# Performance work log

Hardware: AMD Instinct MI355X
Metric: run time of the kernel (lower is better)

## Reference

```python
import jax, jax.numpy as jnp
import numpy as np
from jax import lax

NEG = -1e30  # safe -inf surrogate (avoids nan grads)
CTC_WEIGHT = 0.3


def _excl_cumsum(e):
    # exclusive cumsum along last axis: (..., U) -> (..., U+1)
    c = jnp.cumsum(e, axis=-1)
    return jnp.concatenate([jnp.zeros_like(c[..., :1]), c], axis=-1)


def _rnnt_loss(log_probs, targets, frame_len, tgt_len, blank):
    """RNNT forward DP. log_probs: (B,T,U+1,V) log-softmaxed. Returns per-seq NLL (B,)."""
    B, T, U1, V = log_probs.shape
    blank_lp = log_probs[..., blank]  # (B,T,U1)
    emit = jnp.take_along_axis(log_probs[:, :, :U1 - 1, :],
                               targets[:, None, :, None], axis=3)[..., 0]  # (B,T,U)
    # alpha[0,u] = sum_{j<u} emit[0,j]
    alpha0 = _excl_cumsum(emit[:, 0])  # (B,U1)

    def step(alpha_prev, inp):
        blank_prev, emit_t = inp  # (B,U1), (B,U)
        a = alpha_prev + blank_prev
        # alpha[t,u] = LSE(a_u, alpha[t,u-1] + emit[t,u-1]) solved in closed form:
        # alpha[t,u] = E[u] + cumLSE_{k<=u}(a_k - E[k]),  E = exclusive cumsum of emit
        E = _excl_cumsum(emit_t)
        alpha_t = E + lax.associative_scan(jnp.logaddexp, a - E, axis=-1)
        return alpha_t, alpha_t

    xs = (jnp.swapaxes(blank_lp[:, :-1], 0, 1), jnp.swapaxes(emit[:, 1:], 0, 1))
    _, alphas = lax.scan(step, alpha0, xs)
    alphas = jnp.concatenate([alpha0[None], alphas], axis=0)  # (T,B,U1)
    bi = jnp.arange(B)
    t_idx = frame_len - 1
    ll = alphas[t_idx, bi, tgt_len] + blank_lp[bi, t_idx, tgt_len]
    return -ll


def _ctc_loss(log_probs, targets, frame_len, tgt_len, blank):
    """CTC forward DP. log_probs: (B,T,V) log-softmaxed. Returns per-seq NLL (B,)."""
    B, T, V = log_probs.shape
    U = targets.shape[1]
    S = 2 * U + 1
    ext = jnp.full((B, S), blank, dtype=targets.dtype).at[:, 1::2].set(targets)  # (B,S)
    lp_ext = jnp.take_along_axis(log_probs, ext[:, None, :], axis=2)  # (B,T,S)
    ext_m2 = jnp.pad(ext[:, :-2], ((0, 0), (2, 0)), constant_values=blank)
    can_skip = (jnp.arange(S)[None, :] >= 2) & (ext != blank) & (ext != ext_m2)
    alpha0 = jnp.full((B, S), NEG).at[:, 0].set(lp_ext[:, 0, 0]).at[:, 1].set(lp_ext[:, 0, 1])

    def step(alpha, lp_t):
        p1 = jnp.pad(alpha[:, :-1], ((0, 0), (1, 0)), constant_values=NEG)
        p2 = jnp.where(can_skip,
                       jnp.pad(alpha[:, :-2], ((0, 0), (2, 0)), constant_values=NEG), NEG)
        m = jnp.maximum(jnp.maximum(alpha, p1), p2)
        new = lp_t + m + jnp.log(jnp.exp(alpha - m) + jnp.exp(p1 - m) + jnp.exp(p2 - m))
        return new, new

    _, alphas = lax.scan(step, alpha0, jnp.swapaxes(lp_ext, 0, 1)[1:])
    alphas = jnp.concatenate([alpha0[None], alphas], axis=0)  # (T,B,S)
    bi = jnp.arange(B)
    t_idx = frame_len - 1
    a_last = alphas[t_idx, bi, 2 * tgt_len]
    a_prev = alphas[t_idx, bi, 2 * tgt_len - 1]
    return -jnp.logaddexp(a_last, a_prev)


def setup_inputs() -> dict:
    key = jax.random.key(0)
    ks = jax.random.split(key, 9)
    B, T, U, V = 4, 200, 50, 1024
    D, H = 512, 640
    return {
        "x_enc": jax.random.normal(ks[0], (B, T, D), jnp.float32),
        "x_dec": jax.random.normal(ks[1], (B, U + 1, H), jnp.float32),
        "target": jax.random.randint(ks[2], (B, U), 0, V - 1),  # excludes blank = V-1
        "frame_length": jax.random.randint(ks[3], (B,), 150, T + 1).astype(jnp.int32),
        "target_length": jax.random.randint(ks[4], (B,), 30, U + 1).astype(jnp.int32),
        "W_ctc": jax.random.normal(ks[5], (D, V), jnp.float32) * 0.02,
        "b_ctc": jnp.zeros((V,), jnp.float32),
        "W_enc": jax.random.normal(ks[6], (D, H), jnp.float32) * 0.02,
        "W_pred": jax.random.normal(ks[7], (H, H), jnp.float32) * 0.02,
        "b_joint": jnp.zeros((H,), jnp.float32),
        "W_out": jax.random.normal(ks[8], (H, V), jnp.float32) * 0.02,
        "b_out": jnp.zeros((V,), jnp.float32),
    }


def reference(x_enc, x_dec, target, frame_length, target_length,
              W_ctc, b_ctc, W_enc, W_pred, b_joint, W_out, b_out):
    B = x_enc.shape[0]
    V = W_ctc.shape[1]
    blank = V - 1
    # CTC head: linear + log_softmax over vocab
    ctc_lp = jax.nn.log_softmax(x_enc @ W_ctc + b_ctc, axis=-1)  # (B,T,V)
    # Joiner: enc proj (B,T,1,J) + pred proj (B,1,U+1,J) -> tanh -> vocab
    joint = jnp.tanh(jnp.einsum('btd,dj->btj', x_enc, W_enc)[:, :, None, :]
                     + jnp.einsum('buh,hj->buj', x_dec, W_pred)[:, None, :, :]
                     + b_joint)  # (B,T,U+1,J)
    rnnt_lp = jax.nn.log_softmax(jnp.einsum('btuj,jv->btuv', joint, W_out) + b_out, axis=-1)
    rnnt = _rnnt_loss(rnnt_lp, target, frame_length, target_length, blank).mean()
    ctc = _ctc_loss(ctc_lp, target, frame_length, target_length, blank).sum() / B
    return rnnt + CTC_WEIGHT * ctc
```

## Files before the change

kernel.cpp:

```cpp
#include <hip/hip_runtime.h>
#include <hip/hip_bf16.h>

typedef __bf16 bf16_t;
typedef __attribute__((ext_vector_type(8))) __bf16 bf16x8;
typedef __attribute__((ext_vector_type(4))) float f32x4;
typedef __attribute__((ext_vector_type(8))) int i32x8;
typedef __attribute__((ext_vector_type(4))) int i32x4;

#define NEGV (-1e30f)

#define BB 4
#define TT 200
#define UU 50
#define U1 51
#define VV 1024
#define DD 512
#define HH 640
#define RTOT (BB*TT*U1)
#define RPAD 40832
#define NBLK 638
#define SS 101

__device__ __forceinline__ float lae(float a, float b) {
    float mx = fmaxf(a, b);
    return mx + __logf(__expf(a - mx) + __expf(b - mx));
}
__device__ __forceinline__ float lae3(float a, float b, float c) {
    float mx = fmaxf(fmaxf(a, b), c);
    return mx + __logf(__expf(a - mx) + __expf(b - mx) + __expf(c - mx));
}
__device__ __forceinline__ float tanh_fast(float x) {
    float ex = __expf(2.f * x);
    return 1.f - 2.f / (ex + 1.f);
}

__device__ __forceinline__ void pack_seg(const float* __restrict__ W, bf16_t* __restrict__ Wf,
                                         int e, int K32, int N)
{
    int j  = e & 7;
    int l  = (e >> 3) & 63;
    int kk = (e >> 9) % K32;
    int nt = e / (K32 * 512);
    int v = nt * 16 + (l & 15);
    int k = kk * 32 + ((l >> 4) << 2) + (j & 3) + ((j >> 2) << 4);
    Wf[e] = (bf16_t)W[(size_t)k * N + v];
}

__device__ __forceinline__ void pack_out8_mx(const float* __restrict__ W, unsigned* __restrict__ Wf8,
                                             int e32)
{
    int w4   = e32 & 7;
    int l    = (e32 >> 3) & 63;
    int ksnt = e32 >> 9;
    int ks   = ksnt % 5;
    int nt   = ksnt / 5;
    int v = nt * 16 + (l & 15);
    int kb = ks * 128 + ((l >> 4) << 5) + w4 * 4;
    float f[4];
#pragma unroll
    for (int t = 0; t < 4; ++t) f[t] = W[(size_t)(kb + t) * VV + v] * 16.f;
    unsigned r = __builtin_amdgcn_cvt_pk_fp8_f32(f[0], f[1], 0, false);
    r = __builtin_amdgcn_cvt_pk_fp8_f32(f[2], f[3], r, true);
    Wf8[e32] = r;
}

__global__ void pack_all(const float* __restrict__ Wout, const float* __restrict__ Wenc,
                         const float* __restrict__ Wpred, const float* __restrict__ Wctc,
                         unsigned* __restrict__ FOut8, bf16_t* __restrict__ FEnc,
                         bf16_t* __restrict__ FPred, bf16_t* __restrict__ FCtc)
{
    int e = blockIdx.x * 256 + threadIdx.x;
    if (e < 163840) { pack_out8_mx(Wout, FOut8, e); return; }
    e -= 163840;
    if (e < 327680) { pack_seg(Wenc, FEnc, e, 16, 640); return; }
    e -= 327680;
    if (e < 409600) { pack_seg(Wpred, FPred, e, 20, 640); return; }
    e -= 409600;
    pack_seg(Wctc, FCtc, e, 16, 1024);
}

template<int K32, int L, bool LSE, int J>
__device__ void gemm_dev(const float* __restrict__ A, int M, int rowbase, int K,
                         const bf16_t* __restrict__ Wf, const float* __restrict__ bias,
                         float* __restrict__ C, float* __restrict__ lse_out, int N,
                         bf16_t* Atile, float (*ps)[8])
{
    const int tid = threadIdx.x;
#pragma unroll
    for (int it = 0; it < J * K32 / 8; ++it) {
        int fi = it * 512 + tid;
        int l = fi & 63, jk = fi >> 6;
        int j = jk / K32, kk = jk - j * K32;
        int row = rowbase + j * 16 + (l & 15);
        if (row > M - 1) row = M - 1;
        int c0 = kk * 32 + ((l >> 4) << 2);
        const float4 a0 = *(const float4*)&A[(size_t)row * K + c0];
        const float4 a1 = *(const float4*)&A[(size_t)row * K + c0 + 16];
        bf16x8 v;
        v[0] = (bf16_t)a0.x; v[1] = (bf16_t)a0.y; v[2] = (bf16_t)a0.z; v[3] = (bf16_t)a0.w;
        v[4] = (bf16_t)a1.x; v[5] = (bf16_t)a1.y; v[6] = (bf16_t)a1.z; v[7] = (bf16_t)a1.w;
        *(bf16x8*)&Atile[(size_t)fi * 8] = v;
    }
    __syncthreads();

    const int l = tid & 63, w = tid >> 6;
    const int lrow = l & 15, lhi = l >> 4;

    f32x4 acc[J][L];
#pragma unroll
    for (int j = 0; j < J; ++j)
#pragma unroll
        for (int li = 0; li < L; ++li) acc[j][li] = f32x4{0.f, 0.f, 0.f, 0.f};

    for (int kk = 0; kk < K32; ++kk) {
        bf16x8 a[J];
#pragma unroll
        for (int j = 0; j < J; ++j)
            a[j] = *(const bf16x8*)&Atile[(size_t)(((j * K32 + kk) * 64 + l) * 8)];
#pragma unroll
        for (int li = 0; li < L; ++li) {
            bf16x8 b = *(const bf16x8*)&Wf[(size_t)(((w * L + li) * K32 + kk) * 64 + l) * 8];
#pragma unroll
            for (int j = 0; j < J; ++j)
                acc[j][li] = __builtin_amdgcn_mfma_f32_16x16x32_bf16(a[j], b, acc[j][li], 0, 0, 0);
        }
    }

    float se[J][4];
    if (LSE) {
#pragma unroll
        for (int j = 0; j < J; ++j)
#pragma unroll
            for (int i = 0; i < 4; ++i) se[j][i] = 0.f;
    }
#pragma unroll
    for (int j = 0; j < J; ++j)
#pragma unroll
        for (int li = 0; li < L; ++li) {
            int col = (w * L + li) * 16 + lrow;
            float bv = bias ? bias[col] : 0.f;
#pragma unroll
            for (int i = 0; i < 4; ++i) {
                int grow = rowbase + 16 * j + lhi * 4 + i;
                float x = acc[j][li][i] + bv;
                if (grow < M) C[(size_t)grow * N + col] = x;
                if (LSE) se[j][i] += __expf(x);
            }
        }
    if (LSE) {
#pragma unroll
        for (int d = 1; d < 16; d <<= 1)
#pragma unroll
            for (int j = 0; j < J; ++j)
#pragma unroll
                for (int i = 0; i < 4; ++i) se[j][i] += __shfl_xor(se[j][i], d);
        if (lrow == 0) {
#pragma unroll
            for (int j = 0; j < J; ++j)
#pragma unroll
                for (int i = 0; i < 4; ++i) ps[16 * j + lhi * 4 + i][w] = se[j][i];
        }
        __syncthreads();
        if (tid < J * 16) {
            float s = 0.f;
#pragma unroll
            for (int w0 = 0; w0 < 8; ++w0) s += ps[tid][w0];
            int grow = rowbase + tid;
            if (grow < M) lse_out[grow] = __logf(s);
        }
    }
}

__global__ __launch_bounds__(512)
void mfma_gemm3(const float* __restrict__ x_enc, const float* __restrict__ x_dec,
                const bf16_t* __restrict__ FEnc, const bf16_t* __restrict__ FPred,
                const bf16_t* __restrict__ FCtc, const float* __restrict__ b_ctc,
                float* __restrict__ enc_proj, float* __restrict__ pred_proj,
                float* __restrict__ ctc_logits, float* __restrict__ ctc_lse)
{
    __shared__ bf16_t Atile[40960];
    __shared__ float ps[64][8];
    int blk = blockIdx.x;
    if (blk < 13)
        gemm_dev<16, 5, false, 4>(x_enc, 800, blk * 64, 512, FEnc, nullptr, enc_proj, nullptr, 640, Atile, ps);
    else if (blk < 17)
        gemm_dev<20, 5, false, 4>(x_dec, 204, (blk - 13) * 64, 640, FPred, nullptr, pred_proj, nullptr, 640, Atile, ps);
    else
        gemm_dev<16, 8, true, 4>(x_enc, 800, (blk - 17) * 64, 512, FCtc, b_ctc, ctc_logits, ctc_lse, 1024, Atile, ps);
}

__global__ __launch_bounds__(256)
void build_joint(const float* __restrict__ enc, const float* __restrict__ pred,
                 const float* __restrict__ bj, char* __restrict__ FA8)
{
    const int blk = blockIdx.x;
    const int tid = threadIdx.x;
#pragma unroll
    for (int it = 0; it < 10; ++it) {
        int c = it * 256 + tid;
        int lA = c & 63;
        int plane = c >> 6;
        int h = plane & 1;
        int jks = plane >> 1;
        int ks = jks % 5;
        int j = jks / 5;
        int row = j * 16 + (lA & 15);
        int r = blk * 64 + row; if (r > RTOT - 1) r = RTOT - 1;
        int b = r / (TT * U1); int rem = r - b * (TT * U1);
        int t = rem / U1;      int u = rem - t * U1;
        const float* erow = enc + (size_t)(b * TT + t) * HH;
        const float* prow = pred + (size_t)(b * U1 + u) * HH;
        int c0 = ks * 128 + ((lA >> 4) << 5) + h * 16;
        float f[16];
#pragma unroll
        for (int s = 0; s < 4; ++s) {
            int off = c0 + s * 4;
            const float4 e4 = *(const float4*)&erow[off];
            const float4 p4 = *(const float4*)&prow[off];
            const float4 q4 = *(const float4*)&bj[off];
            f[s * 4 + 0] = tanh_fast(e4.x + p4.x + q4.x);
            f[s * 4 + 1] = tanh_fast(e4.y + p4.y + q4.y);
            f[s * 4 + 2] = tanh_fast(e4.z + p4.z + q4.z);
            f[s * 4 + 3] = tanh_fast(e4.w + p4.w + q4.w);
        }
        uint4 v;
        unsigned r0 = __builtin_amdgcn_cvt_pk_fp8_f32(f[0], f[1], 0, false);
        v.x = __builtin_amdgcn_cvt_pk_fp8_f32(f[2], f[3], r0, true);
        r0 = __builtin_amdgcn_cvt_pk_fp8_f32(f[4], f[5], 0, false);
        v.y = __builtin_amdgcn_cvt_pk_fp8_f32(f[6], f[7], r0, true);
        r0 = __builtin_amdgcn_cvt_pk_fp8_f32(f[8], f[9], 0, false);
        v.z = __builtin_amdgcn_cvt_pk_fp8_f32(f[10], f[11], r0, true);
        r0 = __builtin_amdgcn_cvt_pk_fp8_f32(f[12], f[13], 0, false);
        v.w = __builtin_amdgcn_cvt_pk_fp8_f32(f[14], f[15], r0, true);
        *(uint4*)&FA8[(size_t)blk * 40960 + (size_t)c * 16] = v;
    }
}

__global__ __launch_bounds__(512)
void joint_gemm(const char* __restrict__ FA8,
                const unsigned* __restrict__ Wf8,
                const float* __restrict__ bo,
                const int* __restrict__ target,
                float* __restrict__ blank_buf, float* __restrict__ emit_buf)
{
    __shared__ __align__(16) char smbuf[40960];
    char* Afrag8 = smbuf;
    const int tid = threadIdx.x;
    const int blk = blockIdx.x;

    const int l = tid & 63, w = tid >> 6;
    const int lrow = l & 15, lhi = l >> 4;

    const uint4* src = (const uint4*)(FA8 + (size_t)blk * 40960);
#pragma unroll
    for (int it = 0; it < 5; ++it) {
        int c = it * 512 + tid;
        *(uint4*)&Afrag8[(size_t)c * 16] = src[c];
    }
    __syncthreads();

    f32x4 acc[4][8];
#pragma unroll
    for (int j = 0; j < 4; ++j)
#pragma unroll
        for (int li = 0; li < 8; ++li) acc[j][li] = f32x4{0.f, 0.f, 0.f, 0.f};

    const char* Bp8 = (const char*)Wf8 + (size_t)(w * 8) * 10240 + (size_t)l * 32;

    const int rot = blk % 5;
    auto kstep = [&](int ks) {
        i32x8 a[4];
#pragma unroll
        for (int j = 0; j < 4; ++j) {
            i32x4 lo = *(const i32x4*)(Afrag8 + (size_t)(((j * 5 + ks) * 2 + 0) * 1024 + l * 16));
            i32x4 hi = *(const i32x4*)(Afrag8 + (size_t)(((j * 5 + ks) * 2 + 1) * 1024 + l * 16));
            a[j][0] = lo[0]; a[j][1] = lo[1]; a[j][2] = lo[2]; a[j][3] = lo[3];
            a[j][4] = hi[0]; a[j][5] = hi[1]; a[j][6] = hi[2]; a[j][7] = hi[3];
        }
#pragma unroll
        for (int li = 0; li < 8; ++li) {
            i32x8 b = *(const i32x8*)(Bp8 + (size_t)li * 10240 + (size_t)ks * 2048);
#pragma unroll
            for (int j = 0; j < 4; ++j)
                acc[j][li] = __builtin_amdgcn_mfma_scale_f32_16x16x128_f8f6f4(
                    a[j], b, acc[j][li], 0, 0,
                    0, 0x7F7F7F7F, 0, 0x7F7F7F7F);
        }
    };
    for (int ks0 = rot; ks0 < 5; ++ks0) kstep(ks0);
    for (int ks0 = 0; ks0 < rot; ++ks0) kstep(ks0);

    int tg[4][4];
#pragma unroll
    for (int j = 0; j < 4; ++j)
#pragma unroll
        for (int i = 0; i < 4; ++i) {
            int r = blk * 64 + 16 * j + lhi * 4 + i; if (r > RTOT - 1) r = RTOT - 1;
            int b = r / (TT * U1); int rem = r - b * (TT * U1);
            int u = rem % U1;
            tg[j][i] = (u < UU) ? target[b * UU + u] : -1;
        }

    float se[4][4], ee[4][4], bbv[4][4];
#pragma unroll
    for (int j = 0; j < 4; ++j)
#pragma unroll
        for (int i = 0; i < 4; ++i) { se[j][i] = 0.f; ee[j][i] = NEGV; bbv[j][i] = NEGV; }

#pragma unroll
    for (int li = 0; li < 8; ++li) {
        int col = (w * 8 + li) * 16 + lrow;
        float bv = bo[col];
#pragma unroll
        for (int j = 0; j < 4; ++j)
#pragma unroll
            for (int i = 0; i < 4; ++i) {
                float x = acc[j][li][i] * 0.0625f + bv;
                se[j][i] += __expf(x);
                if (col == tg[j][i]) ee[j][i] = x;
            }
    }
    if (w == 7) {
        float bv = bo[1023];
#pragma unroll
        for (int j = 0; j < 4; ++j)
#pragma unroll
            for (int i = 0; i < 4; ++i) {
                float x = acc[j][7][i] * 0.0625f + bv;
                if (lrow == 15) bbv[j][i] = x;
            }
    }
#pragma unroll
    for (int d = 1; d < 16; d <<= 1)
#pragma unroll
        for (int j = 0; j < 4; ++j)
#pragma unroll
            for (int i = 0; i < 4; ++i) {
                se[j][i] += __shfl_xor(se[j][i], d);
                ee[j][i] = fmaxf(ee[j][i], __shfl_xor(ee[j][i], d));
                bbv[j][i] = fmaxf(bbv[j][i], __shfl_xor(bbv[j][i], d));
            }

    __syncthreads();
    float (*ps)[8] = (float (*)[8])(smbuf);
    float (*pe)[8] = (float (*)[8])(smbuf + 2048);
    float (*pb)[8] = (float (*)[8])(smbuf + 4096);
    if (lrow == 0) {
#pragma unroll
        for (int j = 0; j < 4; ++j)
#pragma unroll
            for (int i = 0; i < 4; ++i) {
                int r = 16 * j + lhi * 4 + i;
                ps[r][w] = se[j][i]; pe[r][w] = ee[j][i]; pb[r][w] = bbv[j][i];
            }
    }
    __syncthreads();
    if (tid < 64) {
        float s = 0.f, e = NEGV, bq = NEGV;
#pragma unroll
        for (int w0 = 0; w0 < 8; ++w0) {
            s += ps[tid][w0];
            e = fmaxf(e, pe[tid][w0]);
            bq = fmaxf(bq, pb[tid][w0]);
        }
        float lse = __logf(s);
        int gid = blk * 64 + tid;
        if (gid < RTOT) {
            blank_buf[gid] = bq - lse;
            emit_buf[gid]  = e - lse;
        }
    }
}

__global__ __launch_bounds__(256)
void dp_fused(const float* __restrict__ blank_buf, const float* __restrict__ emit_buf,
              const float* __restrict__ ctc_logits, const float* __restrict__ ctc_lse,
              const int* __restrict__ target, const int* __restrict__ frame_len,
              const int* __restrict__ tgt_len,
              float* __restrict__ out)
{
    __shared__ __align__(16) float sm[28416];
    const int bid = blockIdx.x;
    const int tid = threadIdx.x;

    if (bid < 4) {
        const int b = bid;
        float2* pk = (float2*)sm;
        for (int i = tid; i < TT * U1; i += 256) {
            int t = i / U1, uu = i - t * U1;
            float bl = blank_buf[(b * TT + t) * U1 + uu];
            float em = emit_buf[(b * TT + t) * U1 + uu];
            pk[uu * 217 + t + 8] = make_float2(bl, em);
        }
        __syncthreads();
        if (tid >= 64) return;
        const int u = tid;
        const int fl = frame_len[b], tl = tgt_len[b];
        const int dh = fl - 1 + tl;
        const bool isTL = (u == tl);
        const bool act = (u < U1);
        float A = (u == 0) ? 0.f : NEGV;
        float Asave = (dh == 0 && isTL) ? A : NEGV;
        const float2* prow = pk + u * 217;

        for (int d0 = 1; d0 <= 249; d0 += 8) {
            int tb = d0 - 1 - u;
            int tc = tb; if (tc < -8) tc = -8; if (tc > 200) tc = 200;
            float2 buf[8];
#pragma unroll
            for (int s = 0; s < 8; ++s) buf[s] = prow[tc + 8 + s];
#pragma unroll
            for (int s = 0; s < 8; ++s) {
                int d = d0 + s;
                int t_new = d - u;
                float2 be = buf[s];
                float vshare = A + be.y;
                float left = __shfl_up(vshare, 1);
                if (u == 0) left = NEGV;
                float up = (t_new >= 1) ? (A + be.x) : NEGV;
                float Anew = lae(up, left);
                bool valid = act && (t_new >= 0) && (t_new < TT);
                A = valid ? Anew : A;
                Asave = (isTL && d == dh) ? A : Asave;
            }
        }
        if (isTL && act) {
            float bl = prow[(fl - 1) + 8].x;
            atomicAdd(out, -0.25f * (Asave + bl));
        }
    } else {
        const int b = bid - 4;
        float* lpE = sm;
        float* lpO = sm + 208;
        for (int i = tid; i < TT; i += 256) {
            int bt = b * TT + i;
            lpE[i] = ctc_logits[(size_t)bt * VV + (VV - 1)] - ctc_lse[bt];
        }
        for (int i = tid; i < TT * UU; i += 256) {
            int t = i / UU, uu = i - t * UU;
            int bt = b * TT + t;
            lpO[uu * 209 + t] = ctc_logits[(size_t)bt * VV + target[b * UU + uu]] - ctc_lse[bt];
        }
        __syncthreads();
        if (tid >= 64) return;
        const int u = tid;
        const int fl = frame_len[b], tl = tgt_len[b];
        const bool acte = (u <= 50);
        const bool acto = (u < 50);
        bool skip = (u >= 1 && u < UU) ? (target[b * UU + u] != target[b * UU + u - 1]) : false;
        const float* orow = lpO + u * 209;
        float old_e = (u == 0) ? lpE[0] : NEGV;
        float old_o = (u == 0) ? orow[0] : NEGV;
        float Esave = (fl == 1) ? old_e : NEGV;
        float Osave = (fl == 1) ? old_o : NEGV;

        for (int t0 = 1; t0 <= 193; t0 += 8) {
            float bo8[8], be8[8];
#pragma unroll
            for (int s = 0; s < 8; ++s) { bo8[s] = orow[t0 + s]; be8[s] = lpE[t0 + s]; }
#pragma unroll
            for (int s = 0; s < 8; ++s) {
                int t = t0 + s;
                float prev_o = __shfl_up(old_o, 1);
                if (u == 0) prev_o = NEGV;
                float ne = be8[s] + lae(old_e, prev_o);
                float no = bo8[s] + lae3(old_o, old_e, skip ? prev_o : NEGV);
                old_e = acte ? ne : NEGV;
                old_o = acto ? no : NEGV;
                bool hv = (t == fl - 1) && (t < TT);
                Esave = hv ? old_e : Esave;
                Osave = hv ? old_o : Osave;
            }
        }
        float a_last = __shfl(Esave, tl);
        float a_prev = __shfl(Osave, tl - 1);
        if (u == 0) atomicAdd(out, -0.075f * lae(a_last, a_prev));
    }
}

extern "C" void kernel_launch(void* const* d_in, const int* in_sizes, int n_in,
                              void* d_out, int out_size, void* d_ws, size_t ws_size,
                              hipStream_t stream)
{
    const float* x_enc   = (const float*)d_in[0];
    const float* x_dec   = (const float*)d_in[1];
    const int*   target  = (const int*)d_in[2];
    const int*   frame_l = (const int*)d_in[3];
    const int*   tgt_l   = (const int*)d_in[4];
    const float* W_ctc   = (const float*)d_in[5];
    const float* b_ctc   = (const float*)d_in[6];
    const float* W_enc   = (const float*)d_in[7];
    const float* W_pred  = (const float*)d_in[8];
    const float* b_joint = (const float*)d_in[9];
    const float* W_out   = (const float*)d_in[10];
    const float* b_out   = (const float*)d_in[11];
    float* out = (float*)d_out;

    float* wsf        = (float*)d_ws;
    float* enc_proj   = wsf;
    float* pred_proj  = wsf + 512000;
    float* ctc_logits = wsf + 642560;
    float* ctc_lse    = wsf + 1461760;
    float* blank_buf  = wsf + 1462592;
    float* emit_buf   = wsf + 1503424;
    unsigned* FOut8 = (unsigned*)(wsf + 1544272);
    bf16_t* FEnc  = (bf16_t*)(wsf + 1708112);
    bf16_t* FPred = (bf16_t*)(wsf + 1871952);
    bf16_t* FCtc  = (bf16_t*)(wsf + 2076752);
    char*   FA8   = (char*)(wsf + 2338896);

    hipMemsetAsync(out, 0, sizeof(float), stream);
    pack_all<<<5568, 256, 0, stream>>>(W_out, W_enc, W_pred, W_ctc, FOut8, FEnc, FPred, FCtc);
    mfma_gemm3<<<30, 512, 0, stream>>>(x_enc, x_dec, FEnc, FPred, FCtc, b_ctc,
                                       enc_proj, pred_proj, ctc_logits, ctc_lse);
    build_joint<<<NBLK, 256, 0, stream>>>(enc_proj, pred_proj, b_joint, FA8);
    joint_gemm<<<NBLK, 512, 0, stream>>>(FA8, FOut8, b_out, target, blank_buf, emit_buf);
    dp_fused<<<8, 256, 0, stream>>>(blank_buf, emit_buf, ctc_logits, ctc_lse,
                                    target, frame_l, tgt_l, out);
}
```

Measured before the change: 170.2 us.

## Stage joint tanh tile in LDS with coalesced row loads before fragment swizzle

build_joint now reads enc/pred rows with consecutive threads covering consecutive columns (coalesced float4 loads), computes tanh and fp8-packs into a padded LDS tile, then reads fragment-ordered 16-byte chunks from LDS to write the swizzled output. Row base pointers are precomputed once per block in shared memory. tanh uses a clamped reciprocal-based formula. This removes strided global reads and repeated index divisions, at the cost of about 42KB of LDS and two barriers per block.

```diff
diff --git a/kernel.cpp b/kernel.cpp
--- a/kernel.cpp
+++ b/kernel.cpp
@@ -32,6 +32,12 @@
 __device__ __forceinline__ float tanh_fast(float x) {
     float ex = __expf(2.f * x);
     return 1.f - 2.f / (ex + 1.f);
+}
+__device__ __forceinline__ float tanh_rcp(float x) {
+    x = fminf(fmaxf(x, -10.f), 10.f);
+    float ex = __expf(2.f * x);
+    float r = __builtin_amdgcn_rcpf(ex + 1.f);
+    return (ex - 1.f) * r;
 }
 
 __device__ __forceinline__ void pack_seg(const float* __restrict__ W, bf16_t* __restrict__ Wf,
@@ -193,8 +199,40 @@
 void build_joint(const float* __restrict__ enc, const float* __restrict__ pred,
                  const float* __restrict__ bj, char* __restrict__ FA8)
 {
+    __shared__ __align__(16) char tile[64 * 656];
+    __shared__ const float* ep[64];
+    __shared__ const float* pp[64];
     const int blk = blockIdx.x;
     const int tid = threadIdx.x;
+
+    if (tid < 64) {
+        int r = blk * 64 + tid; if (r > RTOT - 1) r = RTOT - 1;
+        int b = r / (TT * U1); int rem = r - b * (TT * U1);
+        int t = rem / U1;      int u = rem - t * U1;
+        ep[tid] = enc + (size_t)(b * TT + t) * HH;
+        pp[tid] = pred + (size_t)(b * U1 + u) * HH;
+    }
+    __syncthreads();
+
+#pragma unroll 4
+    for (int it = 0; it < 40; ++it) {
+        int i = it * 256 + tid;
+        int row = i / 160;
+        int c4 = i - row * 160;
+        int c0 = c4 * 4;
+        const float4 e4 = *(const float4*)&ep[row][c0];
+        const float4 p4 = *(const float4*)&pp[row][c0];
+        const float4 q4 = *(const float4*)&bj[c0];
+        float f0 = tanh_rcp(e4.x + p4.x + q4.x);
+        float f1 = tanh_rcp(e4.y + p4.y + q4.y);
+        float f2 = tanh_rcp(e4.z + p4.z + q4.z);
+        float f3 = tanh_rcp(e4.w + p4.w + q4.w);
+        unsigned r0 = __builtin_amdgcn_cvt_pk_fp8_f32(f0, f1, 0, false);
+        unsigned v = __builtin_amdgcn_cvt_pk_fp8_f32(f2, f3, r0, true);
+        *(unsigned*)&tile[row * 656 + c0] = v;
+    }
+    __syncthreads();
+
 #pragma unroll
     for (int it = 0; it < 10; ++it) {
         int c = it * 256 + tid;
@@ -205,33 +243,8 @@
         int ks = jks % 5;
         int j = jks / 5;
         int row = j * 16 + (lA & 15);
-        int r = blk * 64 + row; if (r > RTOT - 1) r = RTOT - 1;
-        int b = r / (TT * U1); int rem = r - b * (TT * U1);
-        int t = rem / U1;      int u = rem - t * U1;
-        const float* erow = enc + (size_t)(b * TT + t) * HH;
-        const float* prow = pred + (size_t)(b * U1 + u) * HH;
-        int c0 = ks * 128 + ((lA >> 4) << 5) + h * 16;
-        float f[16];
-#pragma unroll
-        for (int s = 0; s < 4; ++s) {
-            int off = c0 + s * 4;
-            const float4 e4 = *(const float4*)&erow[off];
-            const float4 p4 = *(const float4*)&prow[off];
-            const float4 q4 = *(const float4*)&bj[off];
-            f[s * 4 + 0] = tanh_fast(e4.x + p4.x + q4.x);
-            f[s * 4 + 1] = tanh_fast(e4.y + p4.y + q4.y);
-            f[s * 4 + 2] = tanh_fast(e4.z + p4.z + q4.z);
-            f[s * 4 + 3] = tanh_fast(e4.w + p4.w + q4.w);
-        }
-        uint4 v;
-        unsigned r0 = __builtin_amdgcn_cvt_pk_fp8_f32(f[0], f[1], 0, false);
-        v.x = __builtin_amdgcn_cvt_pk_fp8_f32(f[2], f[3], r0, true);
-        r0 = __builtin_amdgcn_cvt_pk_fp8_f32(f[4], f[5], 0, false);
-        v.y = __builtin_amdgcn_cvt_pk_fp8_f32(f[6], f[7], r0, true);
-        r0 = __builtin_amdgcn_cvt_pk_fp8_f32(f[8], f[9], 0, false);
-        v.z = __builtin_amdgcn_cvt_pk_fp8_f32(f[10], f[11], r0, true);
-        r0 = __builtin_amdgcn_cvt_pk_fp8_f32(f[12], f[13], 0, false);
-        v.w = __builtin_amdgcn_cvt_pk_fp8_f32(f[14], f[15], r0, true);
+        int kbase = ks * 128 + ((lA >> 4) << 5) + h * 16;
+        uint4 v = *(const uint4*)&tile[row * 656 + kbase];
         *(uint4*)&FA8[(size_t)blk * 40960 + (size_t)c * 16] = v;
     }
 }
```

Result: faster. 164.5 us (-3.3%).
